# Kernel tuning notes

Hardware: AMD Instinct MI355X
Metric: run time of the kernel (lower is better)

Reference implementation:

```python
import jax, jax.numpy as jnp
import numpy as np

B, T, D = 4, 2048, 1024
H = 16            # n_heads
DH = D // H       # head dim
E = 8             # n_micro_experts
DE = 256          # micro_expert_dim
TOP_K = 2
EPS = 1e-5


def _ln(x, g, b):
    m = jnp.mean(x, axis=-1, keepdims=True)
    v = jnp.mean(jnp.square(x - m), axis=-1, keepdims=True)
    return (x - m) * jax.lax.rsqrt(v + EPS) * g + b


def setup_inputs() -> dict:
    key = jax.random.key(0)
    ks = jax.random.split(key, 12)
    s = 0.02
    return {
        "x": jax.random.normal(ks[0], (B, T, D), dtype=jnp.float32),
        "ln1_g": jnp.ones((D,), jnp.float32),
        "ln1_b": jnp.zeros((D,), jnp.float32),
        "in_proj_w": jax.random.normal(ks[1], (3 * D, D), jnp.float32) * s,
        "in_proj_b": jnp.zeros((3 * D,), jnp.float32),
        "out_proj_w": jax.random.normal(ks[2], (D, D), jnp.float32) * s,
        "out_proj_b": jnp.zeros((D,), jnp.float32),
        "ln2_g": jnp.ones((D,), jnp.float32),
        "ln2_b": jnp.zeros((D,), jnp.float32),
        "router_w": jax.random.normal(ks[3], (E, D), jnp.float32) * s,
        "log_temp": jnp.zeros((), jnp.float32),
        "Wg": jax.random.normal(ks[4], (E, DE, D), jnp.float32) * s,  # gate proj per expert
        "Wu": jax.random.normal(ks[5], (E, DE, D), jnp.float32) * s,  # up proj per expert
        "Wd": jax.random.normal(ks[6], (E, D, DE), jnp.float32) * s,  # down proj per expert
    }


def reference(x, ln1_g, ln1_b, in_proj_w, in_proj_b, out_proj_w, out_proj_b,
              ln2_g, ln2_b, router_w, log_temp, Wg, Wu, Wd):
    # --- self-attention block (nn.MultiheadAttention, batch_first, no mask) ---
    h = _ln(x, ln1_g, ln1_b)
    qkv = h @ in_proj_w.T + in_proj_b                       # [B,T,3D]
    q, k, v = jnp.split(qkv, 3, axis=-1)
    q = q.reshape(B, T, H, DH).transpose(0, 2, 1, 3)        # [B,H,T,DH]
    k = k.reshape(B, T, H, DH).transpose(0, 2, 1, 3)
    v = v.reshape(B, T, H, DH).transpose(0, 2, 1, 3)
    scores = jnp.einsum("bhqd,bhkd->bhqk", q, k) / np.sqrt(DH).astype(np.float32)
    attn = jax.nn.softmax(scores, axis=-1)
    o = jnp.einsum("bhqk,bhkd->bhqd", attn, v)              # [B,H,T,DH]
    o = o.transpose(0, 2, 1, 3).reshape(B, T, D)
    x = x + o @ out_proj_w.T + out_proj_b

    # --- MicroExpert MoE (soft top-k via sigmoid suppression, dense experts) ---
    h2 = _ln(x, ln2_g, ln2_b)
    temp = jax.nn.softplus(log_temp) + 0.1
    logits = (h2 @ router_w.T) / temp                       # [B,T,E]
    top_vals, _ = jax.lax.top_k(logits, TOP_K)
    threshold = jax.lax.stop_gradient(top_vals[..., -1:])   # k-th largest, detached
    suppression = jax.nn.sigmoid(10.0 * (logits - threshold))
    weights = jax.nn.softmax(logits * suppression, axis=-1)  # [B,T,E]

    hg = jnp.einsum("btd,efd->btef", h2, Wg)                # [B,T,E,DE]
    hu = jnp.einsum("btd,efd->btef", h2, Wu)
    act = jax.nn.silu(hg) * hu
    out_e = jnp.einsum("btef,edf->bted", act, Wd)           # [B,T,E,D]
    moe = jnp.einsum("bted,bte->btd", out_e, weights)
    return x + moe
```

## Files before the change

### kernel.cpp

```cpp
#include <hip/hip_runtime.h>
#include <hip/hip_bf16.h>
#include <cstddef>
#include <cstdint>

constexpr int Bc  = 4;
constexpr int Tc  = 2048;
constexpr int Dc  = 1024;
constexpr int Hc  = 16;
constexpr int Ec  = 8;
constexpr int DEc = 256;
constexpr int NTOK = Bc * Tc;
constexpr int EDE = Ec * DEc;

typedef __attribute__((ext_vector_type(8)))  short  s8v;
typedef __attribute__((ext_vector_type(4)))  float  f4v;
typedef __attribute__((ext_vector_type(16))) float  f16v;
typedef __attribute__((ext_vector_type(8)))  ushort u8v;
typedef __attribute__((ext_vector_type(4)))  ushort u4v;

constexpr float LOG2E = 1.44269504088896340736f;

__device__ inline ushort f2bf(float f) {
  union { float f; uint32_t u; } v; v.f = f;
  uint32_t r = v.u + 0x7FFFu + ((v.u >> 16) & 1u);
  return (ushort)(r >> 16);
}
__device__ inline float exp2v(float x) {
  float r; asm("v_exp_f32 %0, %1" : "=v"(r) : "v"(x)); return r;
}
__device__ inline float max3f(float a, float b, float c) {
  return fmaxf(fmaxf(a, b), c);
}
__device__ inline float pmax32(float x) {
  float a = x, b = x;
  asm("v_permlane32_swap_b32 %0, %1" : "+v"(b), "+v"(a));
  return fmaxf(a, b);
}
__device__ inline float psum32(float x) {
  float a = x, b = x;
  asm("v_permlane32_swap_b32 %0, %1" : "+v"(b), "+v"(a));
  return a + b;
}

#define GLOAD_LDS(gsrc, ldst)                                        \
  __builtin_amdgcn_global_load_lds(                                  \
      (const __attribute__((address_space(1))) void*)(gsrc),         \
      (__attribute__((address_space(3))) void*)(ldst), 16, 0, 0)

__device__ inline uint32_t cvtpk(float a, float b) {
  uint32_t r;
  asm("v_cvt_pk_bf16_f32 %0, %1, %2" : "=v"(r) : "v"(a), "v"(b));
  return r;
}

__device__ inline u8v pack8(const float4& a, const float4& b) {
  u8v o;
  o[0] = f2bf(a.x); o[1] = f2bf(a.y); o[2] = f2bf(a.z); o[3] = f2bf(a.w);
  o[4] = f2bf(b.x); o[5] = f2bf(b.y); o[6] = f2bf(b.z); o[7] = f2bf(b.w);
  return o;
}

__global__ __launch_bounds__(256)
void convert_all(const float* __restrict__ in_w, const float* __restrict__ out_w,
                 const float* __restrict__ Wg, const float* __restrict__ Wu,
                 const float* __restrict__ Wd,
                 ushort* __restrict__ wb_in, ushort* __restrict__ wb_out,
                 ushort* __restrict__ wb_gu, ushort* __restrict__ wb_d) {
  const int b = blockIdx.x;
  const int tid = threadIdx.x;
  if (b < 1536) {
    const size_t i = ((size_t)b * 256 + tid) * 8;
    *(u8v*)(wb_in + i) = pack8(*(const float4*)(in_w + i),
                               *(const float4*)(in_w + i + 4));
  } else if (b < 2048) {
    const size_t i = ((size_t)(b - 1536) * 256 + tid) * 8;
    *(u8v*)(wb_out + i) = pack8(*(const float4*)(out_w + i),
                                *(const float4*)(out_w + i + 4));
  } else if (b < 4096) {
    const size_t i = ((size_t)(b - 2048) * 256 + tid) * 8;
    const int r = (int)(i >> 10), k = (int)(i & 1023);
    const int j = ((r >> 5) << 4) + (r & 15);
    const float* src = (r & 16) ? Wu : Wg;
    *(u8v*)(wb_gu + i) = pack8(*(const float4*)(src + (size_t)j * Dc + k),
                               *(const float4*)(src + (size_t)j * Dc + k + 4));
  } else {
    const size_t i = ((size_t)(b - 4096) * 256 + tid) * 8;
    const int e = (int)(i >> 18);
    const int d = (int)((i >> 8) & 1023);
    const int f = (int)(i & 255);
    *(u8v*)(wb_d + (size_t)d * EDE + e * DEc + f) =
        pack8(*(const float4*)(Wd + i), *(const float4*)(Wd + i + 4));
  }
}

template <int ROUTER>
__global__ __launch_bounds__(256)
void ln_kernel(const float* __restrict__ in, const float* __restrict__ g,
               const float* __restrict__ bt, ushort* __restrict__ out,
               const float* __restrict__ rw, const float* __restrict__ log_temp,
               float* __restrict__ wts) {
  const int row = blockIdx.x;
  const int tid = threadIdx.x;
  const float* xr = in + (size_t)row * Dc;
  float4 v = *(const float4*)(xr + tid * 4);
  float s  = v.x + v.y + v.z + v.w;
  float ss = v.x * v.x + v.y * v.y + v.z * v.z + v.w * v.w;
#pragma unroll
  for (int off = 32; off; off >>= 1) {
    s  += __shfl_xor(s, off);
    ss += __shfl_xor(ss, off);
  }
  __shared__ float red[8];
  const int w = tid >> 6;
  if ((tid & 63) == 0) { red[w] = s; red[4 + w] = ss; }
  __syncthreads();
  const float ts  = red[0] + red[1] + red[2] + red[3];
  const float tss = red[4] + red[5] + red[6] + red[7];
  const float mean = ts * (1.0f / Dc);
  const float var  = tss * (1.0f / Dc) - mean * mean;
  const float rstd = rsqrtf(var + 1e-5f);
  float4 gv = *(const float4*)(g + tid * 4);
  float4 bv = *(const float4*)(bt + tid * 4);
  const float n0 = (v.x - mean) * rstd * gv.x + bv.x;
  const float n1 = (v.y - mean) * rstd * gv.y + bv.y;
  const float n2 = (v.z - mean) * rstd * gv.z + bv.z;
  const float n3 = (v.w - mean) * rstd * gv.w + bv.w;
  u4v o;
  o[0] = f2bf(n0); o[1] = f2bf(n1); o[2] = f2bf(n2); o[3] = f2bf(n3);
  *(u4v*)(out + (size_t)row * Dc + tid * 4) = o;
  if constexpr (ROUTER) {
    float part[Ec];
#pragma unroll
    for (int e = 0; e < Ec; ++e) {
      float4 wv = *(const float4*)(rw + (size_t)e * Dc + tid * 4);
      part[e] = n0 * wv.x + n1 * wv.y + n2 * wv.z + n3 * wv.w;
    }
#pragma unroll
    for (int off = 32; off; off >>= 1) {
#pragma unroll
      for (int e = 0; e < Ec; ++e) part[e] += __shfl_xor(part[e], off);
    }
    __shared__ float red2[4][Ec];
    if ((tid & 63) == 0) {
#pragma unroll
      for (int e = 0; e < Ec; ++e) red2[w][e] = part[e];
    }
    __syncthreads();
    if (tid == 0) {
      const float lt = *log_temp;
      const float temp = log1pf(__expf(lt)) + 0.1f;
      float lg[Ec];
#pragma unroll
      for (int e = 0; e < Ec; ++e)
        lg[e] = (red2[0][e] + red2[1][e] + red2[2][e] + red2[3][e]) / temp;
      float m1 = -1e30f, m2 = -1e30f;
#pragma unroll
      for (int e = 0; e < Ec; ++e) {
        const float vv = lg[e];
        if (vv > m1) { m2 = m1; m1 = vv; }
        else if (vv > m2) { m2 = vv; }
      }
      float sl[Ec];
      float mx = -1e30f;
#pragma unroll
      for (int e = 0; e < Ec; ++e) {
        const float sup = 1.f / (1.f + __expf(-10.f * (lg[e] - m2)));
        sl[e] = lg[e] * sup;
        mx = fmaxf(mx, sl[e]);
      }
      float ssum = 0.f;
#pragma unroll
      for (int e = 0; e < Ec; ++e) {
        const float p = __expf(sl[e] - mx);
        sl[e] = p;
        ssum += p;
      }
      const float inv = 1.f / ssum;
#pragma unroll
      for (int e = 0; e < Ec; ++e) wts[(size_t)row * Ec + e] = sl[e] * inv;
    }
  }
}

template <int EPI>
__global__ __launch_bounds__(512, 2)
void gemm256(const ushort* __restrict__ A, int lda,
             const ushort* __restrict__ B,
             const float* __restrict__ bias,
             void* __restrict__ Cout, int K) {
  __shared__ __align__(16) ushort Asm[2][256 * 64];
  __shared__ __align__(16) ushort Bsm[2][256 * 64];
  const int tid = threadIdx.x;
  const int lane = tid & 63, w = tid >> 6;
  const int g = lane >> 4, c = lane & 15;
  const int wr = w >> 2, wc = w & 3;
  int bid = blockIdx.y * gridDim.x + blockIdx.x;
  const int qq = (gridDim.x * gridDim.y) >> 3;
  bid = (bid & 7) * qq + (bid >> 3);
  const int m0 = (bid / gridDim.x) * 256, n0 = (bid % gridDim.x) * 256;
  f4v acc[8][4];
#pragma unroll
  for (int i = 0; i < 8; ++i)
#pragma unroll
    for (int j = 0; j < 4; ++j) acc[i][j] = f4v{0.f, 0.f, 0.f, 0.f};

  const int srow = tid >> 3;
  const int koff = 8 * ((tid & 7) ^ (srow & 7));

#define STAGE_A(buf, kt, i)                                                  \
  GLOAD_LDS(A + (size_t)(m0 + (i) * 64 + srow) * lda + (kt) * 64 + koff,     \
            &Asm[buf][((i) * 512 + tid) * 8])
#define STAGE_B(buf, kt, i)                                                  \
  GLOAD_LDS(B + (size_t)(n0 + (i) * 64 + srow) * K + (kt) * 64 + koff,       \
            &Bsm[buf][((i) * 512 + tid) * 8])

#define RD_A(buf, mi, ks)                                                    \
  (*(const s8v*)&Asm[buf][(wr * 128 + (mi) * 16 + c) * 64 +                  \
      8 * (((ks) * 4 + g) ^ ((wr * 128 + (mi) * 16 + c) & 7))])
#define RD_B(buf, ni, ks)                                                    \
  (*(const s8v*)&Bsm[buf][(wc * 64 + (ni) * 16 + c) * 64 +                   \
      8 * (((ks) * 4 + g) ^ ((wc * 64 + (ni) * 16 + c) & 7))])

  const int NT = K >> 6;
  STAGE_B(0, 0, 0); STAGE_B(0, 0, 1); STAGE_B(0, 0, 2); STAGE_B(0, 0, 3);
  STAGE_A(0, 0, 0); STAGE_A(0, 0, 2); STAGE_A(0, 0, 1); STAGE_A(0, 0, 3);
  asm volatile("s_waitcnt vmcnt(0)" ::: "memory");
  __builtin_amdgcn_s_barrier();

  for (int t = 0; t < NT; ++t) {
    const int cur = t & 1, nxt = cur ^ 1;
    const bool st = (t + 1 < NT);
    s8v bf[2][4], af[2][2];
#pragma unroll
    for (int ks = 0; ks < 2; ++ks) {
#pragma unroll
      for (int ni = 0; ni < 4; ++ni) bf[ks][ni] = RD_B(cur, ni, ks);
      af[ks][0] = RD_A(cur, 0, ks); af[ks][1] = RD_A(cur, 1, ks);
    }
    if (st) { STAGE_B(nxt, t + 1, 0); STAGE_B(nxt, t + 1, 1); }
    __builtin_amdgcn_s_barrier();
    __builtin_amdgcn_s_setprio(1);
#pragma unroll
    for (int ks = 0; ks < 2; ++ks)
#pragma unroll
      for (int q = 0; q < 2; ++q)
#pragma unroll
        for (int ni = 0; ni < 4; ++ni)
          acc[q][ni] = __builtin_amdgcn_mfma_f32_16x16x32_bf16(
              af[ks][q], bf[ks][ni], acc[q][ni], 0, 0, 0);
    __builtin_amdgcn_s_setprio(0);
    __builtin_amdgcn_s_barrier();
#pragma unroll
    for (int ks = 0; ks < 2; ++ks) {
      af[ks][0] = RD_A(cur, 2, ks); af[ks][1] = RD_A(cur, 3, ks);
    }
    if (st) { STAGE_B(nxt, t + 1, 2); STAGE_B(nxt, t + 1, 3); }
    __builtin_amdgcn_s_barrier();
    __builtin_amdgcn_s_setprio(1);
#pragma unroll
    for (int ks = 0; ks < 2; ++ks)
#pragma unroll
      for (int q = 0; q < 2; ++q)
#pragma unroll
        for (int ni = 0; ni < 4; ++ni)
          acc[2 + q][ni] = __builtin_amdgcn_mfma_f32_16x16x32_bf16(
              af[ks][q], bf[ks][ni], acc[2 + q][ni], 0, 0, 0);
    __builtin_amdgcn_s_setprio(0);
    if (st) asm volatile("s_waitcnt vmcnt(4)" ::: "memory");
    else    asm volatile("s_waitcnt vmcnt(0)" ::: "memory");
    __builtin_amdgcn_s_barrier();
#pragma unroll
    for (int ks = 0; ks < 2; ++ks) {
      af[ks][0] = RD_A(cur, 4, ks); af[ks][1] = RD_A(cur, 5, ks);
    }
    if (st) { STAGE_A(nxt, t + 1, 0); STAGE_A(nxt, t + 1, 2); }
    __builtin_amdgcn_s_barrier();
    __builtin_amdgcn_s_setprio(1);
#pragma unroll
    for (int ks = 0; ks < 2; ++ks)
#pragma unroll
      for (int q = 0; q < 2; ++q)
#pragma unroll
        for (int ni = 0; ni < 4; ++ni)
          acc[4 + q][ni] = __builtin_amdgcn_mfma_f32_16x16x32_bf16(
              af[ks][q], bf[ks][ni], acc[4 + q][ni], 0, 0, 0);
    __builtin_amdgcn_s_setprio(0);
    __builtin_amdgcn_s_barrier();
#pragma unroll
    for (int ks = 0; ks < 2; ++ks) {
      af[ks][0] = RD_A(cur, 6, ks); af[ks][1] = RD_A(cur, 7, ks);
    }
    if (st) { STAGE_A(nxt, t + 1, 1); STAGE_A(nxt, t + 1, 3); }
    __builtin_amdgcn_s_barrier();
    __builtin_amdgcn_s_setprio(1);
#pragma unroll
    for (int ks = 0; ks < 2; ++ks)
#pragma unroll
      for (int q = 0; q < 2; ++q)
#pragma unroll
        for (int ni = 0; ni < 4; ++ni)
          acc[6 + q][ni] = __builtin_amdgcn_mfma_f32_16x16x32_bf16(
              af[ks][q], bf[ks][ni], acc[6 + q][ni], 0, 0, 0);
    __builtin_amdgcn_s_setprio(0);
    if (st) asm volatile("s_waitcnt vmcnt(2)" ::: "memory");
    __builtin_amdgcn_s_barrier();
  }
#undef STAGE_A
#undef STAGE_B
#undef RD_A
#undef RD_B

#pragma unroll
  for (int mi = 0; mi < 8; ++mi) {
    if constexpr (EPI == 4) {
#pragma unroll
      for (int nip = 0; nip < 2; ++nip) {
        const int jbase = ((n0 + wc * 64) >> 1) + nip * 16;
        const int e = jbase >> 8;
#pragma unroll
        for (int j = 0; j < 4; ++j) {
          const int row = m0 + wr * 128 + mi * 16 + g * 4 + j;
          const float wgt = bias[(size_t)row * Ec + e];
          const float gv = acc[mi][2 * nip][j];
          const float uv = acc[mi][2 * nip + 1][j];
          const float av = (gv / (1.f + __expf(-gv))) * uv * wgt;
          ((ushort*)Cout)[(size_t)row * EDE + jbase + c] = f2bf(av);
        }
      }
    } else {
#pragma unroll
      for (int ni = 0; ni < 4; ++ni) {
        const int col = n0 + wc * 64 + ni * 16 + c;
        const int which = col >> 10, hh = (col >> 6) & 15, d = col & 63;
        const int row0 = m0 + wr * 128 + mi * 16 + g * 4;
        const int b = row0 >> 11, t0 = row0 & 2047;
        const float bs = bias[col];
        ushort* base = (ushort*)Cout;
        if (which == 2) {
          u4v pk;
#pragma unroll
          for (int j = 0; j < 4; ++j) pk[j] = f2bf(acc[mi][ni][j] + bs);
          *(u4v*)&base[2 * (size_t)NTOK * Dc +
                       (((size_t)(b * Hc + hh)) * 64 + d) * Tc + t0] = pk;
        } else {
          const float qs = (which == 0) ? 0.125f * LOG2E : 1.f;
          const size_t off = (size_t)which * ((size_t)NTOK * Dc);
#pragma unroll
          for (int j = 0; j < 4; ++j)
            base[off + (((size_t)(b * Hc + hh)) * Tc + t0 + j) * 64 + d] =
                f2bf((acc[mi][ni][j] + bs) * qs);
        }
      }
    }
  }
}

template <int EPI>
__global__ __launch_bounds__(256)
void gemm_bf16(const ushort* __restrict__ A, int lda,
               const ushort* __restrict__ B,
               const float* __restrict__ bias, const float* __restrict__ resid,
               void* __restrict__ Cout, int ldc, int K) {
  __shared__ __align__(16) ushort As[2][128 * 32];
  __shared__ __align__(16) ushort Bs[2][128 * 32];
  const int tid = threadIdx.x;
  const int lane = tid & 63, w = tid >> 6;
  const int g = lane >> 4, c = lane & 15;
  int bid = blockIdx.y * gridDim.x + blockIdx.x;
  const int qq = (gridDim.x * gridDim.y) >> 3;
  bid = (bid & 7) * qq + (bid >> 3);
  const int m0 = (bid / gridDim.x) * 128, n0 = (bid % gridDim.x) * 128;
  const int wm = (w >> 1) * 64, wn = (w & 1) * 64;
  f4v acc[4][4];
#pragma unroll
  for (int i = 0; i < 4; ++i)
#pragma unroll
    for (int j = 0; j < 4; ++j) acc[i][j] = f4v{0.f, 0.f, 0.f, 0.f};

  int srow[2], skoff[2];
#pragma unroll
  for (int seg = 0; seg < 2; ++seg) {
    const int ci = seg * 256 + tid;
    srow[seg] = ci >> 2;
    skoff[seg] = 8 * ((ci & 3) ^ ((srow[seg] >> 1) & 3));
  }
  auto stage = [&](int buf, int k0) {
#pragma unroll
    for (int seg = 0; seg < 2; ++seg) {
      const int ci = seg * 256 + tid;
      GLOAD_LDS(A + (size_t)(m0 + srow[seg]) * lda + k0 + skoff[seg],
                &As[buf][ci * 8]);
      GLOAD_LDS(B + (size_t)(n0 + srow[seg]) * K + k0 + skoff[seg],
                &Bs[buf][ci * 8]);
    }
  };

  stage(0, 0);
  int curb = 0;
  for (int k0 = 0; k0 < K; k0 += 32) {
    const bool st = (k0 + 32 < K);
    if (st) {
      stage(curb ^ 1, k0 + 32);
      asm volatile("s_waitcnt vmcnt(4)" ::: "memory");
    } else {
      asm volatile("s_waitcnt vmcnt(0)" ::: "memory");
    }
    __builtin_amdgcn_s_barrier();
    s8v af[4], bf[4];
#pragma unroll
    for (int mi = 0; mi < 4; ++mi) {
      const int R = wm + mi * 16 + c;
      af[mi] = *(const s8v*)&As[curb][R * 32 + 8 * (g ^ ((R >> 1) & 3))];
    }
#pragma unroll
    for (int ni = 0; ni < 4; ++ni) {
      const int R = wn + ni * 16 + c;
      bf[ni] = *(const s8v*)&Bs[curb][R * 32 + 8 * (g ^ ((R >> 1) & 3))];
    }
    __builtin_amdgcn_s_setprio(1);
#pragma unroll
    for (int mi = 0; mi < 4; ++mi)
#pragma unroll
      for (int ni = 0; ni < 4; ++ni)
        acc[mi][ni] = __builtin_amdgcn_mfma_f32_16x16x32_bf16(
            af[mi], bf[ni], acc[mi][ni], 0, 0, 0);
    __builtin_amdgcn_s_setprio(0);
    __builtin_amdgcn_s_barrier();
    curb ^= 1;
  }

#pragma unroll
  for (int mi = 0; mi < 4; ++mi) {
#pragma unroll
    for (int ni = 0; ni < 4; ++ni) {
#pragma unroll
      for (int j = 0; j < 4; ++j) {
        const int row = m0 + wm + mi * 16 + g * 4 + j;
        const int col = n0 + wn + ni * 16 + c;
        float v = acc[mi][ni][j];
        if constexpr (EPI == 1) {
          v += bias[col] + resid[(size_t)row * ldc + col];
          ((float*)Cout)[(size_t)row * ldc + col] = v;
        } else {
          ((float*)Cout)[(size_t)row * ldc + col] += v;
        }
      }
    }
  }
}

__global__ __launch_bounds__(256)
void attn_mfma(const ushort* __restrict__ Qb, const ushort* __restrict__ Kb,
               const ushort* __restrict__ Vt, ushort* __restrict__ Ob) {
  __shared__ __align__(16) ushort Ksm[2][64 * 64];
  __shared__ __align__(16) ushort Vtsm[2][64 * 64];
  const int tid = threadIdx.x;
  const int lane = tid & 63, w = tid >> 6;
  const int ql = lane & 31, hi = lane >> 5;
  int bid = blockIdx.x;
  bid = (bid & 7) * 128 + (bid >> 3);
  const int qt = bid & 15, bh = bid >> 4;
  const ushort* Qh = Qb + (size_t)bh * Tc * 64;
  const ushort* Kh = Kb + (size_t)bh * Tc * 64;
  const ushort* Vth = Vt + (size_t)bh * 64 * Tc;
  const int qrow = qt * 128 + w * 32 + ql;
  s8v qf[4];
#pragma unroll
  for (int ds = 0; ds < 4; ++ds)
    qf[ds] = *(const s8v*)(Qh + (size_t)qrow * 64 + ds * 16 + hi * 8);
  f16v accO0, accO1;
#pragma unroll
  for (int i = 0; i < 16; ++i) { accO0[i] = 0.f; accO1[i] = 0.f; }
  float mold = -1e30f, lsum = 0.f;
  int srow[2], soff[2];
#pragma unroll
  for (int seg = 0; seg < 2; ++seg) {
    const int ci = seg * 256 + tid;
    srow[seg] = ci >> 3;
    soff[seg] = ((ci & 7) * 8) ^ ((srow[seg] & 7) << 3);
  }
  auto stage = [&](int buf, int j0) {
#pragma unroll
    for (int seg = 0; seg < 2; ++seg) {
      const int ci = seg * 256 + tid;
      GLOAD_LDS(Kh + (size_t)(j0 + srow[seg]) * 64 + soff[seg], &Ksm[buf][ci * 8]);
      GLOAD_LDS(Vth + (size_t)srow[seg] * Tc + j0 + soff[seg], &Vtsm[buf][ci * 8]);
    }
  };

  stage(0, 0);
  int cur = 0;
  for (int j0 = 0; j0 < Tc; j0 += 64) {
    const bool st = (j0 + 64 < Tc);
    if (st) {
      stage(cur ^ 1, j0 + 64);
      asm volatile("s_waitcnt vmcnt(4)" ::: "memory");
    } else {
      asm volatile("s_waitcnt vmcnt(0)" ::: "memory");
    }
    __builtin_amdgcn_s_barrier();
    f16v s0, s1;
#pragma unroll
    for (int i = 0; i < 16; ++i) { s0[i] = 0.f; s1[i] = 0.f; }
    __builtin_amdgcn_s_setprio(1);
#pragma unroll
    for (int ds = 0; ds < 4; ++ds) {
      const int col = (ds * 16 + hi * 8);
      const int r0 = ql;
      s8v kf0 = *(const s8v*)&Ksm[cur][r0 * 64 + (col ^ ((r0 & 7) << 3))];
      s0 = __builtin_amdgcn_mfma_f32_32x32x16_bf16(kf0, qf[ds], s0, 0, 0, 0);
      const int r1 = 32 + ql;
      s8v kf1 = *(const s8v*)&Ksm[cur][r1 * 64 + (col ^ ((r1 & 7) << 3))];
      s1 = __builtin_amdgcn_mfma_f32_32x32x16_bf16(kf1, qf[ds], s1, 0, 0, 0);
    }
    __builtin_amdgcn_s_setprio(0);
    float cc0 = fmaxf(s0[0], s1[0]), cc1 = fmaxf(s0[1], s1[1]);
    float cc2 = fmaxf(s0[2], s1[2]), cc3 = fmaxf(s0[3], s1[3]);
#pragma unroll
    for (int i = 4; i < 16; i += 4) {
      cc0 = max3f(cc0, s0[i + 0], s1[i + 0]);
      cc1 = max3f(cc1, s0[i + 1], s1[i + 1]);
      cc2 = max3f(cc2, s0[i + 2], s1[i + 2]);
      cc3 = max3f(cc3, s0[i + 3], s1[i + 3]);
    }
    float mx = pmax32(fmaxf(max3f(cc0, cc1, cc2), cc3));
    const bool need = mx > mold + 11.5416f;
    if (__any((int)need)) {
      const float mnew = fmaxf(mold, mx);
      const float sc = exp2v(mold - mnew);
      lsum *= sc;
#pragma unroll
      for (int i = 0; i < 16; ++i) { accO0[i] *= sc; accO1[i] *= sc; }
      mold = mnew;
    }
    float r0s = 0.f, r1s = 0.f, r2s = 0.f, r3s = 0.f;
#pragma unroll
    for (int i = 0; i < 16; i += 4) {
      s0[i+0] = exp2v(s0[i+0] - mold); r0s += s0[i+0];
      s0[i+1] = exp2v(s0[i+1] - mold); r1s += s0[i+1];
      s0[i+2] = exp2v(s0[i+2] - mold); r2s += s0[i+2];
      s0[i+3] = exp2v(s0[i+3] - mold); r3s += s0[i+3];
      s1[i+0] = exp2v(s1[i+0] - mold); r0s += s1[i+0];
      s1[i+1] = exp2v(s1[i+1] - mold); r1s += s1[i+1];
      s1[i+2] = exp2v(s1[i+2] - mold); r2s += s1[i+2];
      s1[i+3] = exp2v(s1[i+3] - mold); r3s += s1[i+3];
    }
    lsum += psum32((r0s + r1s) + (r2s + r3s));
    s8v pa[4];
#pragma unroll
    for (int s = 0; s < 4; ++s) {
      const f16v st2 = (s < 2) ? s0 : s1;
      const int mA = 2 * (s & 1);
      uint32_t a0 = cvtpk(st2[4 * mA + 0], st2[4 * mA + 1]);
      uint32_t a1 = cvtpk(st2[4 * mA + 2], st2[4 * mA + 3]);
      uint32_t b0 = cvtpk(st2[4 * mA + 4], st2[4 * mA + 5]);
      uint32_t b1 = cvtpk(st2[4 * mA + 6], st2[4 * mA + 7]);
      asm("v_permlane32_swap_b32 %0, %1" : "+v"(b0), "+v"(a0));
      asm("v_permlane32_swap_b32 %0, %1" : "+v"(b1), "+v"(a1));
      union { uint32_t u[4]; s8v v; } pk;
      pk.u[0] = a0; pk.u[1] = a1; pk.u[2] = b0; pk.u[3] = b1;
      pa[s] = pk.v;
    }
    __builtin_amdgcn_s_setprio(1);
#pragma unroll
    for (int s = 0; s < 4; ++s) {
      const int col = (s * 16 + hi * 8);
      const int r0 = ql;
      s8v vf0 = *(const s8v*)&Vtsm[cur][r0 * 64 + (col ^ ((r0 & 7) << 3))];
      accO0 = __builtin_amdgcn_mfma_f32_32x32x16_bf16(vf0, pa[s], accO0, 0, 0, 0);
      const int r1 = 32 + ql;
      s8v vf1 = *(const s8v*)&Vtsm[cur][r1 * 64 + (col ^ ((r1 & 7) << 3))];
      accO1 = __builtin_amdgcn_mfma_f32_32x32x16_bf16(vf1, pa[s], accO1, 0, 0, 0);
    }
    __builtin_amdgcn_s_setprio(0);
    __builtin_amdgcn_s_barrier();
    cur ^= 1;
  }
  const int h = bh & 15, b = bh >> 4;
  const int tok = b * Tc + qt * 128 + w * 32 + ql;
  const float inv = 1.f / lsum;
  ushort* orow = Ob + (size_t)tok * Dc + h * 64;
#pragma unroll
  for (int dt = 0; dt < 2; ++dt) {
    const f16v ac = dt ? accO1 : accO0;
#pragma unroll
    for (int rq = 0; rq < 4; ++rq) {
      u4v pk;
#pragma unroll
      for (int j = 0; j < 4; ++j) pk[j] = f2bf(ac[4 * rq + j] * inv);
      *(u4v*)&orow[dt * 32 + 8 * rq + 4 * hi] = pk;
    }
  }
}

extern "C" void kernel_launch(void* const* d_in, const int* in_sizes, int n_in,
                              void* d_out, int out_size, void* d_ws, size_t ws_size,
                              hipStream_t stream) {
  (void)in_sizes; (void)n_in; (void)out_size; (void)ws_size;
  const float* x        = (const float*)d_in[0];
  const float* ln1_g    = (const float*)d_in[1];
  const float* ln1_b    = (const float*)d_in[2];
  const float* in_w     = (const float*)d_in[3];
  const float* in_b     = (const float*)d_in[4];
  const float* out_w    = (const float*)d_in[5];
  const float* out_b    = (const float*)d_in[6];
  const float* ln2_g    = (const float*)d_in[7];
  const float* ln2_b    = (const float*)d_in[8];
  const float* rw       = (const float*)d_in[9];
  const float* log_temp = (const float*)d_in[10];
  const float* Wg       = (const float*)d_in[11];
  const float* Wu       = (const float*)d_in[12];
  const float* Wd       = (const float*)d_in[13];
  float* out = (float*)d_out;

  ushort* h_bf   = (ushort*)d_ws;
  ushort* Qb     = h_bf   + (size_t)NTOK * Dc;
  ushort* Kb     = Qb     + (size_t)NTOK * Dc;
  ushort* Vt     = Kb     + (size_t)NTOK * Dc;
  ushort* Ob     = Vt     + (size_t)NTOK * Dc;
  ushort* act    = Ob     + (size_t)NTOK * Dc;
  ushort* wb_in  = act    + (size_t)NTOK * EDE;
  ushort* wb_out = wb_in  + (size_t)3 * Dc * Dc;
  ushort* wb_gu  = wb_out + (size_t)Dc * Dc;
  ushort* wb_d   = wb_gu  + (size_t)2 * EDE * Dc;
  float*  wts    = (float*)(wb_d + (size_t)Dc * EDE);

  const dim3 blk(256);

  convert_all<<<dim3(5120), blk, 0, stream>>>(
      in_w, out_w, Wg, Wu, Wd, wb_in, wb_out, wb_gu, wb_d);

  ln_kernel<0><<<dim3(NTOK), blk, 0, stream>>>(x, ln1_g, ln1_b, h_bf,
                                               nullptr, nullptr, nullptr);
  gemm256<0><<<dim3(3 * Dc / 256, NTOK / 256), dim3(512), 0, stream>>>(
      h_bf, Dc, wb_in, in_b, Qb, Dc);
  attn_mfma<<<dim3(Bc * Hc * (Tc / 128)), blk, 0, stream>>>(Qb, Kb, Vt, Ob);
  gemm_bf16<1><<<dim3(Dc / 128, NTOK / 128), blk, 0, stream>>>(
      Ob, Dc, wb_out, out_b, x, out, Dc, Dc);
  ln_kernel<1><<<dim3(NTOK), blk, 0, stream>>>(out, ln2_g, ln2_b, h_bf,
                                               rw, log_temp, wts);
  gemm256<4><<<dim3(2 * EDE / 256, NTOK / 256), dim3(512), 0, stream>>>(
      h_bf, Dc, wb_gu, wts, act, Dc);
  gemm_bf16<3><<<dim3(Dc / 128, NTOK / 128), blk, 0, stream>>>(
      act, EDE, wb_d, nullptr, nullptr, out, Dc, EDE);
}
```

Measured before the change: 402.9 us.

## Software-pipeline attention: overlap next QK^T with current softmax and PV

Moves the attention inner loop to a triple-buffered K/V ring in shared memory. The QK^T MFMAs for chunk j+1 are issued before the softmax and PV of chunk j, so matrix work can overlap the exp and max VALU work. The cost is more LDS (three buffers instead of two) and more live accumulator registers (two score tiles), which may lower occupancy or cause spills.

```diff
diff --git a/kernel.cpp b/kernel.cpp
--- a/kernel.cpp
+++ b/kernel.cpp
@@ -452,8 +452,8 @@
 __global__ __launch_bounds__(256)
 void attn_mfma(const ushort* __restrict__ Qb, const ushort* __restrict__ Kb,
                const ushort* __restrict__ Vt, ushort* __restrict__ Ob) {
-  __shared__ __align__(16) ushort Ksm[2][64 * 64];
-  __shared__ __align__(16) ushort Vtsm[2][64 * 64];
+  __shared__ __align__(16) ushort Ksm[3][64 * 64];
+  __shared__ __align__(16) ushort Vtsm[3][64 * 64];
   const int tid = threadIdx.x;
   const int lane = tid & 63, w = tid >> 6;
   const int ql = lane & 31, hi = lane >> 5;
@@ -487,19 +487,7 @@
       GLOAD_LDS(Vth + (size_t)srow[seg] * Tc + j0 + soff[seg], &Vtsm[buf][ci * 8]);
     }
   };
-
-  stage(0, 0);
-  int cur = 0;
-  for (int j0 = 0; j0 < Tc; j0 += 64) {
-    const bool st = (j0 + 64 < Tc);
-    if (st) {
-      stage(cur ^ 1, j0 + 64);
-      asm volatile("s_waitcnt vmcnt(4)" ::: "memory");
-    } else {
-      asm volatile("s_waitcnt vmcnt(0)" ::: "memory");
-    }
-    __builtin_amdgcn_s_barrier();
-    f16v s0, s1;
+  auto qkt = [&](int buf, f16v& s0, f16v& s1) {
 #pragma unroll
     for (int i = 0; i < 16; ++i) { s0[i] = 0.f; s1[i] = 0.f; }
     __builtin_amdgcn_s_setprio(1);
@@ -507,13 +495,15 @@
     for (int ds = 0; ds < 4; ++ds) {
       const int col = (ds * 16 + hi * 8);
       const int r0 = ql;
-      s8v kf0 = *(const s8v*)&Ksm[cur][r0 * 64 + (col ^ ((r0 & 7) << 3))];
+      s8v kf0 = *(const s8v*)&Ksm[buf][r0 * 64 + (col ^ ((r0 & 7) << 3))];
       s0 = __builtin_amdgcn_mfma_f32_32x32x16_bf16(kf0, qf[ds], s0, 0, 0, 0);
       const int r1 = 32 + ql;
-      s8v kf1 = *(const s8v*)&Ksm[cur][r1 * 64 + (col ^ ((r1 & 7) << 3))];
+      s8v kf1 = *(const s8v*)&Ksm[buf][r1 * 64 + (col ^ ((r1 & 7) << 3))];
       s1 = __builtin_amdgcn_mfma_f32_32x32x16_bf16(kf1, qf[ds], s1, 0, 0, 0);
     }
     __builtin_amdgcn_s_setprio(0);
+  };
+  auto smpv = [&](int buf, f16v& s0, f16v& s1) {
     float cc0 = fmaxf(s0[0], s1[0]), cc1 = fmaxf(s0[1], s1[1]);
     float cc2 = fmaxf(s0[2], s1[2]), cc3 = fmaxf(s0[3], s1[3]);
 #pragma unroll
@@ -566,15 +556,52 @@
     for (int s = 0; s < 4; ++s) {
       const int col = (s * 16 + hi * 8);
       const int r0 = ql;
-      s8v vf0 = *(const s8v*)&Vtsm[cur][r0 * 64 + (col ^ ((r0 & 7) << 3))];
+      s8v vf0 = *(const s8v*)&Vtsm[buf][r0 * 64 + (col ^ ((r0 & 7) << 3))];
       accO0 = __builtin_amdgcn_mfma_f32_32x32x16_bf16(vf0, pa[s], accO0, 0, 0, 0);
       const int r1 = 32 + ql;
-      s8v vf1 = *(const s8v*)&Vtsm[cur][r1 * 64 + (col ^ ((r1 & 7) << 3))];
+      s8v vf1 = *(const s8v*)&Vtsm[buf][r1 * 64 + (col ^ ((r1 & 7) << 3))];
       accO1 = __builtin_amdgcn_mfma_f32_32x32x16_bf16(vf1, pa[s], accO1, 0, 0, 0);
     }
     __builtin_amdgcn_s_setprio(0);
-    __builtin_amdgcn_s_barrier();
-    cur ^= 1;
+  };
+
+  constexpr int NCH = Tc / 64;
+  stage(0, 0);
+  stage(1, 64);
+  asm volatile("s_waitcnt vmcnt(4)" ::: "memory");
+  __builtin_amdgcn_s_barrier();
+  f16v s0A, s1A, s0B, s1B;
+  qkt(0, s0A, s1A);
+
+  for (int j = 0; j < NCH; j += 2) {
+    {
+      const int cj = j;
+      const bool stg = (cj + 2 < NCH);
+      if (stg) {
+        stage((cj + 2) % 3, (cj + 2) * 64);
+        asm volatile("s_waitcnt vmcnt(4)" ::: "memory");
+      } else {
+        asm volatile("s_waitcnt vmcnt(0)" ::: "memory");
+      }
+      __builtin_amdgcn_s_barrier();
+      if (cj + 1 < NCH) qkt((cj + 1) % 3, s0B, s1B);
+      smpv(cj % 3, s0A, s1A);
+      __builtin_amdgcn_s_barrier();
+    }
+    {
+      const int cj = j + 1;
+      const bool stg = (cj + 2 < NCH);
+      if (stg) {
+        stage((cj + 2) % 3, (cj + 2) * 64);
+        asm volatile("s_waitcnt vmcnt(4)" ::: "memory");
+      } else {
+        asm volatile("s_waitcnt vmcnt(0)" ::: "memory");
+      }
+      __builtin_amdgcn_s_barrier();
+      if (cj + 1 < NCH) qkt((cj + 1) % 3, s0A, s1A);
+      smpv(cj % 3, s0B, s1B);
+      __builtin_amdgcn_s_barrier();
+    }
   }
   const int h = bh & 15, b = bh >> 4;
   const int tok = b * Tc + qt * 128 + w * 32 + ql;
```

Result: no change. 399.4 us (-0.9%).
